# Optimization experiments

Hardware: AMD Instinct MI355X
Metric: run time of the kernel (lower is better)

The kernel has to match this reference:

```python
import jax, jax.numpy as jnp
import numpy as np

B, S, F = 4, 2048, 256
H, D = 8, 32            # n_heads, width_embedding; H*D == F
LN_EPS = 1e-3           # tf.keras LayerNormalization default epsilon


def setup_inputs() -> dict:
    key = jax.random.key(0)
    ks = jax.random.split(key, 6)
    s = 1.0 / np.sqrt(F)
    return {
        "x": jax.random.normal(ks[0], (B, S, F), dtype=jnp.float32),
        "Wq": jax.random.normal(ks[1], (F, H * D), dtype=jnp.float32) * s,
        "Wk": jax.random.normal(ks[2], (F, H * D), dtype=jnp.float32) * s,
        "Wv": jax.random.normal(ks[3], (F, H * D), dtype=jnp.float32) * s,
        "Wf": jax.random.normal(ks[4], (H * D, F), dtype=jnp.float32) * s,
        "bf": jnp.zeros((F,), dtype=jnp.float32),
    }


def reference(x, Wq, Wk, Wv, Wf, bf):
    # QKV projections (no bias), split heads: [B,S,H*D] -> [B,H,S,D]
    def split(t):
        return t.reshape(B, S, H, D).transpose(0, 2, 1, 3)

    q = split(x @ Wq) / jnp.sqrt(jnp.asarray(H, x.dtype))  # NOTE: module scales by sqrt(n_heads)
    k = split(x @ Wk)
    v = split(x @ Wv)

    scores = jnp.einsum("bhsd,bhtd->bhst", q, k)          # [B,H,S,S]
    attn = jax.nn.softmax(scores, axis=-1)
    ctx = jnp.einsum("bhst,bhtd->bhsd", attn, v)           # [B,H,S,D]

    y = ctx.transpose(0, 2, 1, 3).reshape(B, S, H * D)     # merge heads
    y = jax.nn.relu(y @ Wf + bf)                            # final dense with relu

    # residual + LayerNorm(center=False, scale=False)
    z = x + y
    mean = jnp.mean(z, axis=-1, keepdims=True)
    var = jnp.var(z, axis=-1, keepdims=True)
    return (z - mean) * jax.lax.rsqrt(var + LN_EPS)
```

## Files before the change

### kernel.cpp

```cpp
#include <hip/hip_runtime.h>
#include <math.h>

#define NB 4
#define NS 2048
#define NF 256
#define NH 8
#define ND 32

constexpr float LN_EPS = 1e-3f;
constexpr float QSCALE = 0.35355339059327373f;
constexpr float LOG2E  = 1.4426950408889634f;

typedef __bf16 bf16x8 __attribute__((ext_vector_type(8)));
typedef float f32x4 __attribute__((ext_vector_type(4)));

__global__ __launch_bounds__(256)
void prep_w(const float* __restrict__ Wq, const float* __restrict__ Wk,
            const float* __restrict__ Wv, const float* __restrict__ Wf,
            unsigned short* __restrict__ wt)
{
    __shared__ float tile[64][65];
    const int wid = blockIdx.x;
    const int t = threadIdx.x;
    const int z = wid >> 4;
    const int tl = wid & 15;
    const float* W = (z == 0) ? Wq : (z == 1) ? Wk : (z == 2) ? Wv : Wf;
    const float scale = (z == 0) ? QSCALE * LOG2E : 1.0f;
    const int r0 = (tl >> 2) * 64, c0 = (tl & 3) * 64;
    const int tr = t >> 4, tc4 = (t & 15) * 4;

    #pragma unroll
    for (int p = 0; p < 4; ++p) {
        float4 v = *(const float4*)(W + (size_t)(r0 + tr + p * 16) * NF + c0 + tc4);
        tile[tr + p * 16][tc4 + 0] = v.x;
        tile[tr + p * 16][tc4 + 1] = v.y;
        tile[tr + p * 16][tc4 + 2] = v.z;
        tile[tr + p * 16][tc4 + 3] = v.w;
    }
    __syncthreads();
    #pragma unroll
    for (int p = 0; p < 4; ++p) {
        union { ushort4 u; __bf16 h[4]; } o;
        #pragma unroll
        for (int j = 0; j < 4; ++j)
            o.h[j] = (__bf16)(tile[tc4 + j][tr + p * 16] * scale);
        *(ushort4*)(wt + (size_t)z * 65536 + (size_t)(c0 + tr + p * 16) * NF + r0 + tc4) = o.u;
    }
}

__global__ __launch_bounds__(256)
void qkv_mfma(const float* __restrict__ x, const unsigned short* __restrict__ wt,
              unsigned short* __restrict__ qo, unsigned short* __restrict__ ko,
              unsigned short* __restrict__ vo)
{
    const int z = blockIdx.y;
    unsigned short* out = (z == 0) ? qo : (z == 1) ? ko : vo;
    const unsigned short* W = wt + (size_t)z * 65536;

    const int r0 = blockIdx.x * 64;
    const int t = threadIdx.x;
    const int w = t >> 6, lane = t & 63;
    const int l15 = lane & 15, lhi = lane >> 4;
    const int wr = w >> 1, wc = w & 1;

    f32x4 acc[2][8] = {};

    #pragma unroll 2
    for (int kt = 0; kt < NF; kt += 32) {
        const float* xr0 = x + (size_t)(r0 + wr * 32 + l15) * NF + kt + lhi * 8;
        const float* xr1 = x + (size_t)(r0 + wr * 32 + 16 + l15) * NF + kt + lhi * 8;
        float4 f00 = *(const float4*)xr0;
        float4 f01 = *(const float4*)(xr0 + 4);
        float4 f10 = *(const float4*)xr1;
        float4 f11 = *(const float4*)(xr1 + 4);
        bf16x8 a0, a1;
        a0[0] = (__bf16)f00.x; a0[1] = (__bf16)f00.y; a0[2] = (__bf16)f00.z; a0[3] = (__bf16)f00.w;
        a0[4] = (__bf16)f01.x; a0[5] = (__bf16)f01.y; a0[6] = (__bf16)f01.z; a0[7] = (__bf16)f01.w;
        a1[0] = (__bf16)f10.x; a1[1] = (__bf16)f10.y; a1[2] = (__bf16)f10.z; a1[3] = (__bf16)f10.w;
        a1[4] = (__bf16)f11.x; a1[5] = (__bf16)f11.y; a1[6] = (__bf16)f11.z; a1[7] = (__bf16)f11.w;
        #pragma unroll
        for (int c = 0; c < 8; ++c) {
            bf16x8 b = *(const bf16x8*)(W + (size_t)(wc * 128 + c * 16 + l15) * NF + kt + lhi * 8);
            acc[0][c] = __builtin_amdgcn_mfma_f32_16x16x32_bf16(a0, b, acc[0][c], 0, 0, 0);
            acc[1][c] = __builtin_amdgcn_mfma_f32_16x16x32_bf16(a1, b, acc[1][c], 0, 0, 0);
        }
    }

    #pragma unroll
    for (int i = 0; i < 2; ++i) {
        #pragma unroll
        for (int c = 0; c < 8; ++c) {
            const int col = wc * 128 + c * 16 + l15;
            const int h = col >> 5, d = col & 31;
            const int rowbase = r0 + wr * 32 + i * 16 + lhi * 4;
            const int b = rowbase >> 11, s = rowbase & 2047;
            if (z == 2) {
                union { ushort4 u; __bf16 h4[4]; } o;
                #pragma unroll
                for (int r = 0; r < 4; ++r) o.h4[r] = (__bf16)acc[i][c][r];
                *(ushort4*)(out + ((size_t)(b * NH + h) * ND + d) * NS + s) = o.u;
            } else {
                #pragma unroll
                for (int r = 0; r < 4; ++r) {
                    __bf16 o = (__bf16)acc[i][c][r];
                    out[((size_t)(b * NH + h) * NS + (s + r)) * ND + d] = *(unsigned short*)&o;
                }
            }
        }
    }
}

__global__ __launch_bounds__(256)
void attn_mfma(const unsigned short* __restrict__ q, const unsigned short* __restrict__ k,
               const unsigned short* __restrict__ v, unsigned short* __restrict__ ctxb)
{
    const int bh = blockIdx.x;
    const int s0 = blockIdx.y * 128;
    const int t = threadIdx.x;
    const int w = t >> 6;
    const int lane = t & 63;
    const int l15 = lane & 15;
    const int lhi = lane >> 4;
    const int sx  = l15 & 8;
    const int vd  = w * 8 + (lane >> 3);
    const int vk  = (lane & 7) * 8;
    const int vsx = vd & 8;

    __shared__ unsigned short vt[2][32][72];

    const unsigned short* qb  = q + (size_t)bh * NS * ND;
    const unsigned short* kb  = k + (size_t)bh * NS * ND;
    const unsigned short* vtg = v + (size_t)bh * ND * NS + (size_t)vd * NS;

    const int krow = (l15 >> 2) * 8 + (l15 & 3);
    const unsigned short* kbp = kb + (size_t)krow * ND + lhi * 8;

    bf16x8 qf0 = *(const bf16x8*)(qb + (size_t)(s0 + w * 32 + l15) * ND + lhi * 8);
    bf16x8 qf1 = *(const bf16x8*)(qb + (size_t)(s0 + w * 32 + 16 + l15) * ND + lhi * 8);

    float lp0 = 0.f, lp1 = 0.f;
    f32x4 acc00 = {0.f,0.f,0.f,0.f}, acc01 = {0.f,0.f,0.f,0.f};
    f32x4 acc10 = {0.f,0.f,0.f,0.f}, acc11 = {0.f,0.f,0.f,0.f};

    bf16x8 kf[4];
    kf[0] = *(const bf16x8*)(kbp);
    kf[1] = *(const bf16x8*)(kbp + 128);
    kf[2] = *(const bf16x8*)(kbp + 1024);
    kf[3] = *(const bf16x8*)(kbp + 1152);
    {
        bf16x8 vv = *(const bf16x8*)(vtg + vk);
        *(bf16x8*)&vt[0][vd][vk ^ vsx] = vv;
    }
    __syncthreads();

    int cur = 0;
    #pragma unroll 2
    for (int tI = 0; tI < 32; ++tI) {
        const int ktn = ((tI + 1) & 31) * 64;
        bf16x8 vvn = *(const bf16x8*)(vtg + ktn + vk);
        bf16x8 kn[4];
        kn[0] = *(const bf16x8*)(kbp + (size_t)ktn * ND);
        kn[1] = *(const bf16x8*)(kbp + (size_t)ktn * ND + 128);
        kn[2] = *(const bf16x8*)(kbp + (size_t)ktn * ND + 1024);
        kn[3] = *(const bf16x8*)(kbp + (size_t)ktn * ND + 1152);

        const f32x4 zero = {0.f, 0.f, 0.f, 0.f};
        f32x4 sc0[4], sc1[4];
        __builtin_amdgcn_s_setprio(1);
        #pragma unroll
        for (int f = 0; f < 4; ++f) {
            sc0[f] = __builtin_amdgcn_mfma_f32_16x16x32_bf16(kf[f], qf0, zero, 0, 0, 0);
            sc1[f] = __builtin_amdgcn_mfma_f32_16x16x32_bf16(kf[f], qf1, zero, 0, 0, 0);
        }
        __builtin_amdgcn_s_setprio(0);

        bf16x8 pa00, pa01, pa10, pa11;
        float a0 = 0.f, a1 = 0.f;
        #pragma unroll
        for (int r = 0; r < 4; ++r) {
            float p0 = __builtin_amdgcn_exp2f(sc0[0][r]);
            float p1 = __builtin_amdgcn_exp2f(sc0[1][r]);
            float p2 = __builtin_amdgcn_exp2f(sc0[2][r]);
            float p3 = __builtin_amdgcn_exp2f(sc0[3][r]);
            pa00[r]     = (__bf16)p0;
            pa00[4 + r] = (__bf16)p1;
            pa01[r]     = (__bf16)p2;
            pa01[4 + r] = (__bf16)p3;
            a0 += (p0 + p1) + (p2 + p3);
            float s0_ = __builtin_amdgcn_exp2f(sc1[0][r]);
            float s1_ = __builtin_amdgcn_exp2f(sc1[1][r]);
            float s2_ = __builtin_amdgcn_exp2f(sc1[2][r]);
            float s3_ = __builtin_amdgcn_exp2f(sc1[3][r]);
            pa10[r]     = (__bf16)s0_;
            pa10[4 + r] = (__bf16)s1_;
            pa11[r]     = (__bf16)s2_;
            pa11[4 + r] = (__bf16)s3_;
            a1 += (s0_ + s1_) + (s2_ + s3_);
        }
        lp0 += a0; lp1 += a1;

        const int co0 = (lhi * 8) ^ sx;
        const int co1 = (32 + lhi * 8) ^ sx;
        bf16x8 vfa0 = *(const bf16x8*)&vt[cur][l15][co0];
        bf16x8 vfb0 = *(const bf16x8*)&vt[cur][16 + l15][co0];
        bf16x8 vfa1 = *(const bf16x8*)&vt[cur][l15][co1];
        bf16x8 vfb1 = *(const bf16x8*)&vt[cur][16 + l15][co1];
        __builtin_amdgcn_s_setprio(1);
        acc00 = __builtin_amdgcn_mfma_f32_16x16x32_bf16(pa00, vfa0, acc00, 0, 0, 0);
        acc01 = __builtin_amdgcn_mfma_f32_16x16x32_bf16(pa00, vfb0, acc01, 0, 0, 0);
        acc10 = __builtin_amdgcn_mfma_f32_16x16x32_bf16(pa10, vfa0, acc10, 0, 0, 0);
        acc11 = __builtin_amdgcn_mfma_f32_16x16x32_bf16(pa10, vfb0, acc11, 0, 0, 0);
        acc00 = __builtin_amdgcn_mfma_f32_16x16x32_bf16(pa01, vfa1, acc00, 0, 0, 0);
        acc01 = __builtin_amdgcn_mfma_f32_16x16x32_bf16(pa01, vfb1, acc01, 0, 0, 0);
        acc10 = __builtin_amdgcn_mfma_f32_16x16x32_bf16(pa11, vfa1, acc10, 0, 0, 0);
        acc11 = __builtin_amdgcn_mfma_f32_16x16x32_bf16(pa11, vfb1, acc11, 0, 0, 0);
        __builtin_amdgcn_s_setprio(0);

        *(bf16x8*)&vt[cur ^ 1][vd][vk ^ vsx] = vvn;
        #pragma unroll
        for (int f = 0; f < 4; ++f) kf[f] = kn[f];
        __syncthreads();
        cur ^= 1;
    }

    lp0 += __shfl_xor(lp0, 16);
    lp0 += __shfl_xor(lp0, 32);
    lp1 += __shfl_xor(lp1, 16);
    lp1 += __shfl_xor(lp1, 32);

    const int b = bh >> 3, h = bh & 7;
    #pragma unroll
    for (int r = 0; r < 4; ++r) {
        float inv0 = 1.0f / __shfl(lp0, lhi * 4 + r);
        float inv1 = 1.0f / __shfl(lp1, lhi * 4 + r);
        int row0 = s0 + w * 32 + lhi * 4 + r;
        int row1 = row0 + 16;
        unsigned short* op0 = ctxb + ((size_t)b * NS + row0) * NF + h * ND;
        unsigned short* op1 = ctxb + ((size_t)b * NS + row1) * NF + h * ND;
        __bf16 o00 = (__bf16)(acc00[r] * inv0);
        __bf16 o01 = (__bf16)(acc01[r] * inv0);
        __bf16 o10 = (__bf16)(acc10[r] * inv1);
        __bf16 o11 = (__bf16)(acc11[r] * inv1);
        op0[l15]      = *(unsigned short*)&o00;
        op0[16 + l15] = *(unsigned short*)&o01;
        op1[l15]      = *(unsigned short*)&o10;
        op1[16 + l15] = *(unsigned short*)&o11;
    }
}

__global__ __launch_bounds__(256)
void dense_ln(const unsigned short* __restrict__ ctxb, const unsigned short* __restrict__ wft,
              const float* __restrict__ bfp, const float* __restrict__ x,
              float* __restrict__ out)
{
    const int r0 = blockIdx.x * 32;
    const int t = threadIdx.x;
    const int w = t >> 6;
    const int lane = t & 63;
    const int l15 = lane & 15;
    const int lhi = lane >> 4;

    __shared__ float zs[32][258];

    f32x4 acc[2][4] = {};

    #pragma unroll 2
    for (int kt = 0; kt < NF; kt += 32) {
        bf16x8 a0 = *(const bf16x8*)(ctxb + (size_t)(r0 + l15) * NF + kt + lhi * 8);
        bf16x8 a1 = *(const bf16x8*)(ctxb + (size_t)(r0 + 16 + l15) * NF + kt + lhi * 8);
        #pragma unroll
        for (int c = 0; c < 4; ++c) {
            bf16x8 b = *(const bf16x8*)(wft + (size_t)(w * 64 + c * 16 + l15) * NF + kt + lhi * 8);
            acc[0][c] = __builtin_amdgcn_mfma_f32_16x16x32_bf16(a0, b, acc[0][c], 0, 0, 0);
            acc[1][c] = __builtin_amdgcn_mfma_f32_16x16x32_bf16(a1, b, acc[1][c], 0, 0, 0);
        }
    }

    #pragma unroll
    for (int i = 0; i < 2; ++i) {
        #pragma unroll
        for (int c = 0; c < 4; ++c) {
            const int col = w * 64 + c * 16 + l15;
            const float bb = bfp[col];
            #pragma unroll
            for (int r = 0; r < 4; ++r) {
                const int row = i * 16 + lhi * 4 + r;
                zs[row][col] = fmaxf(acc[i][c][r] + bb, 0.0f);
            }
        }
    }
    __syncthreads();

    #pragma unroll
    for (int i = 0; i < 8; ++i) {
        const int row = w * 8 + i;
        float4 yv = *(const float4*)&zs[row][lane * 4];
        float4 xv = *(const float4*)(x + (size_t)(r0 + row) * NF + lane * 4);
        float z0 = xv.x + yv.x, z1 = xv.y + yv.y;
        float z2 = xv.z + yv.z, z3 = xv.w + yv.w;
        float sum = z0 + z1 + z2 + z3;
        float sq  = z0*z0 + z1*z1 + z2*z2 + z3*z3;
        #pragma unroll
        for (int o = 1; o < 64; o <<= 1) {
            sum += __shfl_xor(sum, o);
            sq  += __shfl_xor(sq, o);
        }
        float mean = sum * (1.0f / NF);
        float var  = sq * (1.0f / NF) - mean * mean;
        float rstd = rsqrtf(var + LN_EPS);
        float4 o4;
        o4.x = (z0 - mean) * rstd;
        o4.y = (z1 - mean) * rstd;
        o4.z = (z2 - mean) * rstd;
        o4.w = (z3 - mean) * rstd;
        *(float4*)(out + (size_t)(r0 + row) * NF + lane * 4) = o4;
    }
}

extern "C" void kernel_launch(void* const* d_in, const int* in_sizes, int n_in,
                              void* d_out, int out_size, void* d_ws, size_t ws_size,
                              hipStream_t stream)
{
    const float* x  = (const float*)d_in[0];
    const float* Wq = (const float*)d_in[1];
    const float* Wk = (const float*)d_in[2];
    const float* Wv = (const float*)d_in[3];
    const float* Wf = (const float*)d_in[4];
    const float* bf = (const float*)d_in[5];
    float* out = (float*)d_out;

    const size_t per = (size_t)NB * NH * NS * ND;
    unsigned short* q    = (unsigned short*)d_ws;
    unsigned short* kk   = q + per;
    unsigned short* vv   = kk + per;
    unsigned short* wt   = vv + per;
    unsigned short* ctxb = wt + 4 * 65536;

    prep_w<<<dim3(64), 256, 0, stream>>>(Wq, Wk, Wv, Wf, wt);
    qkv_mfma<<<dim3(128, 3), 256, 0, stream>>>(x, wt, q, kk, vv);
    attn_mfma<<<dim3(NB * NH, NS / 128), 256, 0, stream>>>(q, kk, vv, ctxb);
    dense_ln<<<dim3((NB * NS) / 32), 256, 0, stream>>>(ctxb, wt + 3 * 65536, bf, x, out);
}
```

Baseline: 77.13 us.

## Fuse QKV projections per block, stage Q/K stores through LDS, widen blocks

The QKV kernel now computes all three projections in one block over 32 rows with 8 waves, so each x tile is loaded and converted once instead of three times. Q and K outputs are staged through shared memory so the head-split stores are coalesced 16-byte writes instead of scattered 2-byte stores. The dense+LayerNorm kernel moves to 512 threads with each wave covering 32 columns. This trades fewer registers per wave and extra barriers for better reuse and store coalescing.

```diff
diff --git a/kernel.cpp b/kernel.cpp
--- a/kernel.cpp
+++ b/kernel.cpp
@@ -48,64 +48,90 @@
     }
 }
 
-__global__ __launch_bounds__(256)
+__global__ __launch_bounds__(512)
 void qkv_mfma(const float* __restrict__ x, const unsigned short* __restrict__ wt,
               unsigned short* __restrict__ qo, unsigned short* __restrict__ ko,
               unsigned short* __restrict__ vo)
 {
-    const int z = blockIdx.y;
-    unsigned short* out = (z == 0) ? qo : (z == 1) ? ko : vo;
-    const unsigned short* W = wt + (size_t)z * 65536;
-
-    const int r0 = blockIdx.x * 64;
+    const int r0 = blockIdx.x * 32;
     const int t = threadIdx.x;
     const int w = t >> 6, lane = t & 63;
     const int l15 = lane & 15, lhi = lane >> 4;
-    const int wr = w >> 1, wc = w & 1;
-
-    f32x4 acc[2][8] = {};
+    const int c0 = w * 32;
+
+    __shared__ unsigned short zs[32][264];
+
+    f32x4 acc[2][2][3] = {};
 
     #pragma unroll 2
     for (int kt = 0; kt < NF; kt += 32) {
-        const float* xr0 = x + (size_t)(r0 + wr * 32 + l15) * NF + kt + lhi * 8;
-        const float* xr1 = x + (size_t)(r0 + wr * 32 + 16 + l15) * NF + kt + lhi * 8;
-        float4 f00 = *(const float4*)xr0;
-        float4 f01 = *(const float4*)(xr0 + 4);
-        float4 f10 = *(const float4*)xr1;
-        float4 f11 = *(const float4*)(xr1 + 4);
-        bf16x8 a0, a1;
-        a0[0] = (__bf16)f00.x; a0[1] = (__bf16)f00.y; a0[2] = (__bf16)f00.z; a0[3] = (__bf16)f00.w;
-        a0[4] = (__bf16)f01.x; a0[5] = (__bf16)f01.y; a0[6] = (__bf16)f01.z; a0[7] = (__bf16)f01.w;
-        a1[0] = (__bf16)f10.x; a1[1] = (__bf16)f10.y; a1[2] = (__bf16)f10.z; a1[3] = (__bf16)f10.w;
-        a1[4] = (__bf16)f11.x; a1[5] = (__bf16)f11.y; a1[6] = (__bf16)f11.z; a1[7] = (__bf16)f11.w;
-        #pragma unroll
-        for (int c = 0; c < 8; ++c) {
-            bf16x8 b = *(const bf16x8*)(W + (size_t)(wc * 128 + c * 16 + l15) * NF + kt + lhi * 8);
-            acc[0][c] = __builtin_amdgcn_mfma_f32_16x16x32_bf16(a0, b, acc[0][c], 0, 0, 0);
-            acc[1][c] = __builtin_amdgcn_mfma_f32_16x16x32_bf16(a1, b, acc[1][c], 0, 0, 0);
-        }
-    }
-
-    #pragma unroll
-    for (int i = 0; i < 2; ++i) {
-        #pragma unroll
-        for (int c = 0; c < 8; ++c) {
-            const int col = wc * 128 + c * 16 + l15;
+        bf16x8 a[2];
+        #pragma unroll
+        for (int ai = 0; ai < 2; ++ai) {
+            const float* xr = x + (size_t)(r0 + ai * 16 + l15) * NF + kt + lhi * 8;
+            float4 f0 = *(const float4*)xr;
+            float4 f1 = *(const float4*)(xr + 4);
+            a[ai][0] = (__bf16)f0.x; a[ai][1] = (__bf16)f0.y;
+            a[ai][2] = (__bf16)f0.z; a[ai][3] = (__bf16)f0.w;
+            a[ai][4] = (__bf16)f1.x; a[ai][5] = (__bf16)f1.y;
+            a[ai][6] = (__bf16)f1.z; a[ai][7] = (__bf16)f1.w;
+        }
+        #pragma unroll
+        for (int z = 0; z < 3; ++z) {
+            const unsigned short* W = wt + (size_t)z * 65536;
+            #pragma unroll
+            for (int cf = 0; cf < 2; ++cf) {
+                bf16x8 b = *(const bf16x8*)(W + (size_t)(c0 + cf * 16 + l15) * NF + kt + lhi * 8);
+                acc[0][cf][z] = __builtin_amdgcn_mfma_f32_16x16x32_bf16(a[0], b, acc[0][cf][z], 0, 0, 0);
+                acc[1][cf][z] = __builtin_amdgcn_mfma_f32_16x16x32_bf16(a[1], b, acc[1][cf][z], 0, 0, 0);
+            }
+        }
+    }
+
+    #pragma unroll
+    for (int ai = 0; ai < 2; ++ai) {
+        #pragma unroll
+        for (int cf = 0; cf < 2; ++cf) {
+            const int col = c0 + cf * 16 + l15;
             const int h = col >> 5, d = col & 31;
-            const int rowbase = r0 + wr * 32 + i * 16 + lhi * 4;
+            const int rowbase = r0 + ai * 16 + lhi * 4;
             const int b = rowbase >> 11, s = rowbase & 2047;
-            if (z == 2) {
-                union { ushort4 u; __bf16 h4[4]; } o;
-                #pragma unroll
-                for (int r = 0; r < 4; ++r) o.h4[r] = (__bf16)acc[i][c][r];
-                *(ushort4*)(out + ((size_t)(b * NH + h) * ND + d) * NS + s) = o.u;
-            } else {
+            union { ushort4 u; __bf16 h4[4]; } o;
+            #pragma unroll
+            for (int r = 0; r < 4; ++r) o.h4[r] = (__bf16)acc[ai][cf][2][r];
+            *(ushort4*)(vo + ((size_t)(b * NH + h) * ND + d) * NS + s) = o.u;
+        }
+    }
+
+    #pragma unroll
+    for (int z = 0; z < 2; ++z) {
+        __syncthreads();
+        #pragma unroll
+        for (int ai = 0; ai < 2; ++ai) {
+            #pragma unroll
+            for (int cf = 0; cf < 2; ++cf) {
+                const int col = c0 + cf * 16 + l15;
                 #pragma unroll
                 for (int r = 0; r < 4; ++r) {
-                    __bf16 o = (__bf16)acc[i][c][r];
-                    out[((size_t)(b * NH + h) * NS + (s + r)) * ND + d] = *(unsigned short*)&o;
+                    __bf16 o = (__bf16)acc[ai][cf][z][r];
+                    zs[ai * 16 + lhi * 4 + r][col] = *(unsigned short*)&o;
                 }
             }
+        }
+        __syncthreads();
+        unsigned short* out = (z == 0) ? qo : ko;
+        #pragma unroll
+        for (int p = 0; p < 2; ++p) {
+            const int row = (t >> 5) + p * 16;
+            const int col8 = (t & 31) * 8;
+            const int h = col8 >> 5, d = col8 & 31;
+            const int gr = r0 + row;
+            const int b = gr >> 11, s = gr & 2047;
+            ushort4 u0 = *(ushort4*)&zs[row][col8];
+            ushort4 u1 = *(ushort4*)&zs[row][col8 + 4];
+            unsigned short* op = out + ((size_t)(b * NH + h) * NS + s) * ND + d;
+            *(ushort4*)op = u0;
+            *(ushort4*)(op + 4) = u1;
         }
     }
 }
@@ -248,7 +274,7 @@
     }
 }
 
-__global__ __launch_bounds__(256)
+__global__ __launch_bounds__(512)
 void dense_ln(const unsigned short* __restrict__ ctxb, const unsigned short* __restrict__ wft,
               const float* __restrict__ bfp, const float* __restrict__ x,
               float* __restrict__ out)
@@ -259,41 +285,42 @@
     const int lane = t & 63;
     const int l15 = lane & 15;
     const int lhi = lane >> 4;
+    const int c0 = w * 32;
 
     __shared__ float zs[32][258];
 
-    f32x4 acc[2][4] = {};
+    f32x4 acc[2][2] = {};
 
     #pragma unroll 2
     for (int kt = 0; kt < NF; kt += 32) {
         bf16x8 a0 = *(const bf16x8*)(ctxb + (size_t)(r0 + l15) * NF + kt + lhi * 8);
         bf16x8 a1 = *(const bf16x8*)(ctxb + (size_t)(r0 + 16 + l15) * NF + kt + lhi * 8);
         #pragma unroll
-        for (int c = 0; c < 4; ++c) {
-            bf16x8 b = *(const bf16x8*)(wft + (size_t)(w * 64 + c * 16 + l15) * NF + kt + lhi * 8);
-            acc[0][c] = __builtin_amdgcn_mfma_f32_16x16x32_bf16(a0, b, acc[0][c], 0, 0, 0);
-            acc[1][c] = __builtin_amdgcn_mfma_f32_16x16x32_bf16(a1, b, acc[1][c], 0, 0, 0);
-        }
-    }
-
-    #pragma unroll
-    for (int i = 0; i < 2; ++i) {
-        #pragma unroll
-        for (int c = 0; c < 4; ++c) {
-            const int col = w * 64 + c * 16 + l15;
+        for (int cf = 0; cf < 2; ++cf) {
+            bf16x8 b = *(const bf16x8*)(wft + (size_t)(c0 + cf * 16 + l15) * NF + kt + lhi * 8);
+            acc[0][cf] = __builtin_amdgcn_mfma_f32_16x16x32_bf16(a0, b, acc[0][cf], 0, 0, 0);
+            acc[1][cf] = __builtin_amdgcn_mfma_f32_16x16x32_bf16(a1, b, acc[1][cf], 0, 0, 0);
+        }
+    }
+
+    #pragma unroll
+    for (int ai = 0; ai < 2; ++ai) {
+        #pragma unroll
+        for (int cf = 0; cf < 2; ++cf) {
+            const int col = c0 + cf * 16 + l15;
             const float bb = bfp[col];
             #pragma unroll
             for (int r = 0; r < 4; ++r) {
-                const int row = i * 16 + lhi * 4 + r;
-                zs[row][col] = fmaxf(acc[i][c][r] + bb, 0.0f);
+                const int row = ai * 16 + lhi * 4 + r;
+                zs[row][col] = fmaxf(acc[ai][cf][r] + bb, 0.0f);
             }
         }
     }
     __syncthreads();
 
     #pragma unroll
-    for (int i = 0; i < 8; ++i) {
-        const int row = w * 8 + i;
+    for (int i = 0; i < 4; ++i) {
+        const int row = w * 4 + i;
         float4 yv = *(const float4*)&zs[row][lane * 4];
         float4 xv = *(const float4*)(x + (size_t)(r0 + row) * NF + lane * 4);
         float z0 = xv.x + yv.x, z1 = xv.y + yv.y;
@@ -337,7 +364,7 @@
     unsigned short* ctxb = wt + 4 * 65536;
 
     prep_w<<<dim3(64), 256, 0, stream>>>(Wq, Wk, Wv, Wf, wt);
-    qkv_mfma<<<dim3(128, 3), 256, 0, stream>>>(x, wt, q, kk, vv);
+    qkv_mfma<<<dim3(256), 512, 0, stream>>>(x, wt, q, kk, vv);
     attn_mfma<<<dim3(NB * NH, NS / 128), 256, 0, stream>>>(q, kk, vv, ctxb);
-    dense_ln<<<dim3((NB * NS) / 32), 256, 0, stream>>>(ctxb, wt + 3 * 65536, bf, x, out);
-}
+    dense_ln<<<dim3((NB * NS) / 32), 512, 0, stream>>>(ctxb, wt + 3 * 65536, bf, x, out);
+}
```

New measurement: 76.01 us, median of 2. No clear change (-1.5%).
